# Kernel tuning notes

Hardware: AMD Instinct MI355X
Metric: run time of the kernel (lower is better)

The kernel has to match this reference:

```python
import jax, jax.numpy as jnp
import numpy as np

N_NODES = 500_000
N_EDGES = 16_000_000
N_TYPES = 64


def setup_inputs() -> dict:
    key = jax.random.key(0)
    ks = jax.random.split(key, 8)
    voltage = jax.random.normal(ks[0], (N_NODES,), dtype=jnp.float32)
    stimulus = jax.random.normal(ks[1], (N_NODES,), dtype=jnp.float32)
    neuron_type = jax.random.randint(ks[2], (N_NODES,), 0, N_TYPES, dtype=jnp.int64)
    edge_index = jax.random.randint(ks[3], (2, N_EDGES), 0, N_NODES, dtype=jnp.int64)
    w = jax.random.normal(ks[4], (N_EDGES,), dtype=jnp.float32)
    V_i_rest = jax.random.normal(ks[5], (N_NODES,), dtype=jnp.float32)
    # tau must be positive (divisor); shift uniform away from zero
    tau_i = jax.random.uniform(ks[6], (N_NODES,), dtype=jnp.float32) + 0.5
    # multiple_ReLU per-type scale, abs(1 + 0.5*randn) as in the module
    type_params = jnp.abs(1.0 + 0.5 * jax.random.normal(ks[7], (N_TYPES, 1), dtype=jnp.float32))
    return {
        "voltage": voltage,
        "stimulus": stimulus,
        "neuron_type": neuron_type,
        "edge_index": edge_index,
        "w": w,
        "V_i_rest": V_i_rest,
        "tau_i": tau_i,
        "type_params": type_params,
    }


def reference(voltage, stimulus, neuron_type, edge_index, w, V_i_rest, tau_i, type_params):
    # voltage: (N,), edge_index: (2,E), w: (E,), type_params: (T,1)
    v = voltage[:, None]  # (N,1)
    src = edge_index[0]
    dst = edge_index[1]
    # per-edge message: w_e * relu(v_src) * param[type(src)]   -> (E,1)
    edge_msg = w[:, None] * jax.nn.relu(v[src]) * type_params[neuron_type[src]]
    # scatter_add to destination nodes -> (N,1)
    msg = jax.ops.segment_sum(edge_msg, dst, num_segments=v.shape[0])
    # dv/dt = (-v + msg + e + v_rest) / tau
    dv = (-v + msg + stimulus[:, None] + V_i_rest[:, None]) / tau_i[:, None]
    return dv
```

## Files before the change

### kernel.cpp

```cpp
#include <hip/hip_runtime.h>


#define BSHIFT 10
#define BSIZE  1024
#define NBMAX  512
#define GPB    4096
#define EPB    (GPB * 4)


__global__ void pre_g_kernel(const float* __restrict__ v,
                             const int* __restrict__ ntype,
                             const float* __restrict__ tp,
                             float* __restrict__ g, int n) {
    int i = blockIdx.x * blockDim.x + threadIdx.x;
    if (i < n) {
        float x = v[i];
        x = x > 0.0f ? x : 0.0f;
        g[i] = x * tp[ntype[i]];
    }
}

__global__ __launch_bounds__(1024, 8)
void scatter_kernel(const int* __restrict__ src,
                    const int* __restrict__ dst,
                    const float* __restrict__ w,
                    const float* __restrict__ g,
                    unsigned* __restrict__ sorted,
                    unsigned* __restrict__ lpref_g,
                    int G, int n_edges, int nblk, int nb) {
    __shared__ unsigned stage[EPB];
    __shared__ unsigned lstart[NBMAX];
    __shared__ unsigned lcur[NBMAX];
    __shared__ unsigned wsum[16];
    int blk = blockIdx.x, tid = threadIdx.x;
    int wid = tid >> 6, lane = tid & 63;
    bool last = (blk == nblk - 1);

    if (tid < NBMAX) lcur[tid] = 0;
    __syncthreads();

    const int4*   s4 = (const int4*)src;
    const int4*   d4 = (const int4*)dst;
    const float4* w4 = (const float4*)w;
    int gstart = blk * GPB;
    int gend = gstart + GPB; if (gend > G) gend = G;

    int4 dreg[4];
    #pragma unroll
    for (int k = 0; k < 4; k++) {
        int i = gstart + tid + k * 1024;
        if (i < gend) {
            int4 d = d4[i];
            dreg[k] = d;
            atomicAdd(&lcur[((unsigned)d.x) >> BSHIFT], 1u);
            atomicAdd(&lcur[((unsigned)d.y) >> BSHIFT], 1u);
            atomicAdd(&lcur[((unsigned)d.z) >> BSHIFT], 1u);
            atomicAdd(&lcur[((unsigned)d.w) >> BSHIFT], 1u);
        }
    }
    if (last) {
        for (int i = G * 4 + tid; i < n_edges; i += 1024)
            atomicAdd(&lcur[((unsigned)dst[i]) >> BSHIFT], 1u);
    }
    __syncthreads();

    unsigned cntv = (tid < NBMAX) ? lcur[tid] : 0u;
    unsigned inc = cntv;
    #pragma unroll
    for (int o = 1; o < 64; o <<= 1) {
        unsigned t = __shfl_up(inc, o, 64);
        if (lane >= o) inc += t;
    }
    if (lane == 63) wsum[wid] = inc;
    __syncthreads();
    if (tid < 64) {
        unsigned x = (lane < 16) ? wsum[lane] : 0u;
        unsigned xi = x;
        #pragma unroll
        for (int o = 1; o < 16; o <<= 1) {
            unsigned t = __shfl_up(xi, o, 64);
            if (lane >= o) xi += t;
        }
        if (lane < 16) wsum[lane] = xi - x;
    }
    __syncthreads();
    if (tid < NBMAX) {
        unsigned excl = inc - cntv + wsum[wid];
        lstart[tid] = excl;
        lcur[tid] = excl;
    }
    __syncthreads();

    #pragma unroll
    for (int k = 0; k < 4; k++) {
        int i = gstart + tid + k * 1024;
        if (i < gend) {
            int4 s = s4[i]; float4 wv = w4[i]; int4 d = dreg[k];
            {
                unsigned b = ((unsigned)d.x) >> BSHIFT;
                unsigned pos = atomicAdd(&lcur[b], 1u);
                stage[pos] = (__float_as_uint(wv.x * g[s.x]) & ~(unsigned)(BSIZE - 1)) |
                             ((unsigned)d.x & (BSIZE - 1));
            }
            {
                unsigned b = ((unsigned)d.y) >> BSHIFT;
                unsigned pos = atomicAdd(&lcur[b], 1u);
                stage[pos] = (__float_as_uint(wv.y * g[s.y]) & ~(unsigned)(BSIZE - 1)) |
                             ((unsigned)d.y & (BSIZE - 1));
            }
            {
                unsigned b = ((unsigned)d.z) >> BSHIFT;
                unsigned pos = atomicAdd(&lcur[b], 1u);
                stage[pos] = (__float_as_uint(wv.z * g[s.z]) & ~(unsigned)(BSIZE - 1)) |
                             ((unsigned)d.z & (BSIZE - 1));
            }
            {
                unsigned b = ((unsigned)d.w) >> BSHIFT;
                unsigned pos = atomicAdd(&lcur[b], 1u);
                stage[pos] = (__float_as_uint(wv.w * g[s.w]) & ~(unsigned)(BSIZE - 1)) |
                             ((unsigned)d.w & (BSIZE - 1));
            }
        }
    }
    if (last) {
        for (int i = G * 4 + tid; i < n_edges; i += 1024) {
            int dd = dst[i];
            unsigned b = ((unsigned)dd) >> BSHIFT;
            unsigned pos = atomicAdd(&lcur[b], 1u);
            stage[pos] = (__float_as_uint(w[i] * g[src[i]]) & ~(unsigned)(BSIZE - 1)) |
                         ((unsigned)dd & (BSIZE - 1));
        }
    }
    __syncthreads();

    unsigned count = (unsigned)(gend > gstart ? (gend - gstart) * 4 : 0) +
                     (last ? (unsigned)(n_edges - G * 4) : 0u);
    uint4* out4 = (uint4*)(sorted + (size_t)blk * EPB);
    const uint4* st4 = (const uint4*)stage;
    unsigned nq = (count + 3u) >> 2;
    for (unsigned i = tid; i < nq; i += 1024) out4[i] = st4[i];

    unsigned* row = lpref_g + (size_t)blk * (nb + 1);
    if (tid < (unsigned)nb)       row[tid] = lstart[tid];
    else if (tid == (unsigned)nb) row[nb]  = count;
}

__global__ __launch_bounds__(512, 8)
void accum_kernel(const unsigned* __restrict__ sorted,
                  const unsigned* __restrict__ lpref_g,
                  const float* __restrict__ v,
                  const float* __restrict__ stim,
                  const float* __restrict__ vrest,
                  const float* __restrict__ tau,
                  float* __restrict__ out,
                  int n_nodes, int nblk, int nb) {
    __shared__ float acc[BSIZE];
    int b = blockIdx.x, tid = threadIdx.x;
    acc[tid] = 0.0f;
    acc[tid + 512] = 0.0f;
    __syncthreads();
    int wave = tid >> 6, lane = tid & 63;
    int rowlen = nb + 1;
    for (int base = wave * 64; base < nblk; base += 8 * 64) {
        int myslice = base + lane;
        unsigned s = 0, e = 0;
        if (myslice < nblk) {
            const unsigned* row = lpref_g + (size_t)myslice * rowlen + b;
            s = row[0];
            e = row[1];
        }
        int kmax = nblk - base; if (kmax > 64) kmax = 64;
        for (int k = 0; k < kmax; k++) {
            unsigned sv = __shfl(s, k, 64);
            unsigned ev = __shfl(e, k, 64);
            const unsigned* seg = sorted + (size_t)(base + k) * EPB;
            for (unsigned j = sv + lane; j < ev; j += 64) {
                unsigned u = seg[j];
                atomicAdd(&acc[u & (BSIZE - 1)],
                          __uint_as_float(u & ~(unsigned)(BSIZE - 1)));
            }
        }
    }
    __syncthreads();
    int i0 = (b << BSHIFT) + tid;
    if (i0 < n_nodes)
        out[i0] = (-v[i0] + acc[tid] + stim[i0] + vrest[i0]) / tau[i0];
    int i1 = i0 + 512;
    if (i1 < n_nodes)
        out[i1] = (-v[i1] + acc[tid + 512] + stim[i1] + vrest[i1]) / tau[i1];
}


__global__ void node_pre_kernel(const float* __restrict__ v,
                                const int* __restrict__ ntype,
                                const float* __restrict__ tp,
                                float* __restrict__ g,
                                float* __restrict__ msg, int n) {
    int i = blockIdx.x * blockDim.x + threadIdx.x;
    if (i < n) {
        float x = v[i];
        x = x > 0.0f ? x : 0.0f;
        g[i] = x * tp[ntype[i]];
        msg[i] = 0.0f;
    }
}

__global__ void edge_scatter_kernel(const int* __restrict__ src,
                                    const int* __restrict__ dst,
                                    const float* __restrict__ w,
                                    const float* __restrict__ g,
                                    float* __restrict__ msg, int n_vec) {
    int i = blockIdx.x * blockDim.x + threadIdx.x;
    if (i < n_vec) {
        int4 s = ((const int4*)src)[i];
        int4 d = ((const int4*)dst)[i];
        float4 wv = ((const float4*)w)[i];
        atomicAdd(&msg[d.x], wv.x * g[s.x]);
        atomicAdd(&msg[d.y], wv.y * g[s.y]);
        atomicAdd(&msg[d.z], wv.z * g[s.z]);
        atomicAdd(&msg[d.w], wv.w * g[s.w]);
    }
}

__global__ void edge_scatter_tail(const int* __restrict__ src,
                                  const int* __restrict__ dst,
                                  const float* __restrict__ w,
                                  const float* __restrict__ g,
                                  float* __restrict__ msg,
                                  int start, int n_edges) {
    int i = start + blockIdx.x * blockDim.x + threadIdx.x;
    if (i < n_edges) atomicAdd(&msg[dst[i]], w[i] * g[src[i]]);
}

__global__ void node_post_kernel(const float* __restrict__ v,
                                 const float* __restrict__ msg,
                                 const float* __restrict__ stim,
                                 const float* __restrict__ vrest,
                                 const float* __restrict__ tau,
                                 float* __restrict__ out, int n) {
    int i = blockIdx.x * blockDim.x + threadIdx.x;
    if (i < n)
        out[i] = (-v[i] + msg[i] + stim[i] + vrest[i]) / tau[i];
}


extern "C" void kernel_launch(void* const* d_in, const int* in_sizes, int n_in,
                              void* d_out, int out_size, void* d_ws, size_t ws_size,
                              hipStream_t stream) {
    const float* voltage  = (const float*)d_in[0];
    const float* stimulus = (const float*)d_in[1];
    const int*   ntype    = (const int*)d_in[2];
    const int*   edge_idx = (const int*)d_in[3];
    const float* w        = (const float*)d_in[4];
    const float* vrest    = (const float*)d_in[5];
    const float* tau      = (const float*)d_in[6];
    const float* tp       = (const float*)d_in[7];
    float* out = (float*)d_out;

    const int n_nodes = in_sizes[0];
    const int n_edges = in_sizes[4];
    const int* src = edge_idx;
    const int* dst = edge_idx + n_edges;

    const int B = 256;
    const int G = n_edges / 4;
    int nblk = (G + GPB - 1) / GPB;
    if (nblk < 1) nblk = 1;
    const int nb = (n_nodes + BSIZE - 1) / BSIZE;

    auto align256 = [](size_t x) { return (x + 255) & ~(size_t)255; };
    size_t g_off      = 0;
    size_t sorted_off = align256(g_off + (size_t)n_nodes * 4);
    size_t lpref_off  = align256(sorted_off + (size_t)nblk * EPB * 4);
    size_t need       = align256(lpref_off + (size_t)nblk * (nb + 1) * 4);

    if (nb < NBMAX && ws_size >= need) {
        float*    g      = (float*)((char*)d_ws + g_off);
        unsigned* sorted = (unsigned*)((char*)d_ws + sorted_off);
        unsigned* lpref  = (unsigned*)((char*)d_ws + lpref_off);

        pre_g_kernel<<<(n_nodes + B - 1) / B, B, 0, stream>>>(
            voltage, ntype, tp, g, n_nodes);
        scatter_kernel<<<nblk, 1024, 0, stream>>>(
            src, dst, w, g, sorted, lpref, G, n_edges, nblk, nb);
        accum_kernel<<<nb, 512, 0, stream>>>(
            sorted, lpref, voltage, stimulus, vrest, tau, out,
            n_nodes, nblk, nb);
    } else {
        float* g   = (float*)d_ws;
        float* msg = (float*)d_ws + n_nodes;
        node_pre_kernel<<<(n_nodes + B - 1) / B, B, 0, stream>>>(
            voltage, ntype, tp, g, msg, n_nodes);
        if (G > 0)
            edge_scatter_kernel<<<(G + B - 1) / B, B, 0, stream>>>(
                src, dst, w, g, msg, G);
        if (G * 4 < n_edges) {
            int rem = n_edges - G * 4;
            edge_scatter_tail<<<(rem + B - 1) / B, B, 0, stream>>>(
                src, dst, w, g, msg, G * 4, n_edges);
        }
        node_post_kernel<<<(n_nodes + B - 1) / B, B, 0, stream>>>(
            voltage, msg, stimulus, vrest, tau, out, n_nodes);
    }
}
```

Measured before the change: 420.8 us.

## Scatter edges into global per-bucket buffers via atomic reservation, simplify accumulation

```diff
diff --git a/kernel.cpp b/kernel.cpp
--- a/kernel.cpp
+++ b/kernel.cpp
@@ -6,18 +6,22 @@
 #define NBMAX  512
 #define GPB    4096
 #define EPB    (GPB * 4)
+#define SPILL_CAP 131072
 
 
 __global__ void pre_g_kernel(const float* __restrict__ v,
                              const int* __restrict__ ntype,
                              const float* __restrict__ tp,
-                             float* __restrict__ g, int n) {
+                             float* __restrict__ g,
+                             unsigned* __restrict__ gcur,
+                             int n, int nb) {
     int i = blockIdx.x * blockDim.x + threadIdx.x;
     if (i < n) {
         float x = v[i];
         x = x > 0.0f ? x : 0.0f;
         g[i] = x * tp[ntype[i]];
     }
+    if (i <= nb) gcur[i] = 0u;
 }
 
 __global__ __launch_bounds__(1024, 8)
@@ -25,12 +29,14 @@
                     const int* __restrict__ dst,
                     const float* __restrict__ w,
                     const float* __restrict__ g,
-                    unsigned* __restrict__ sorted,
-                    unsigned* __restrict__ lpref_g,
-                    int G, int n_edges, int nblk, int nb) {
+                    unsigned* __restrict__ bucketbuf,
+                    unsigned* __restrict__ gcur,
+                    uint2* __restrict__ spill,
+                    int G, int n_edges, int nblk, int nb, int cap) {
     __shared__ unsigned stage[EPB];
     __shared__ unsigned lstart[NBMAX];
     __shared__ unsigned lcur[NBMAX];
+    __shared__ unsigned gposs[NBMAX];
     __shared__ unsigned wsum[16];
     int blk = blockIdx.x, tid = threadIdx.x;
     int wid = tid >> 6, lane = tid & 63;
@@ -133,61 +139,89 @@
     }
     __syncthreads();
 
-    unsigned count = (unsigned)(gend > gstart ? (gend - gstart) * 4 : 0) +
-                     (last ? (unsigned)(n_edges - G * 4) : 0u);
-    uint4* out4 = (uint4*)(sorted + (size_t)blk * EPB);
-    const uint4* st4 = (const uint4*)stage;
-    unsigned nq = (count + 3u) >> 2;
-    for (unsigned i = tid; i < nq; i += 1024) out4[i] = st4[i];
-
-    unsigned* row = lpref_g + (size_t)blk * (nb + 1);
-    if (tid < (unsigned)nb)       row[tid] = lstart[tid];
-    else if (tid == (unsigned)nb) row[nb]  = count;
-}
-
-__global__ __launch_bounds__(512, 8)
-void accum_kernel(const unsigned* __restrict__ sorted,
-                  const unsigned* __restrict__ lpref_g,
+    if (tid < nb) {
+        unsigned len = lcur[tid] - lstart[tid];
+        unsigned p = 0u;
+        if (len) {
+            p = atomicAdd(&gcur[tid], len);
+            if (p + len > (unsigned)cap) {
+                atomicSub(&gcur[tid], len);
+                unsigned sp = atomicAdd(&gcur[nb], len);
+                p = 0x80000000u | sp;
+            }
+        }
+        gposs[tid] = p;
+    }
+    __syncthreads();
+
+    for (int b = wid; b < nb; b += 16) {
+        unsigned st  = lstart[b];
+        unsigned len = lcur[b] - st;
+        if (!len) continue;
+        unsigned p = gposs[b];
+        if (p & 0x80000000u) {
+            unsigned sp = p & 0x7FFFFFFFu;
+            for (unsigned j = lane; j < len; j += 64) {
+                if (sp + j < SPILL_CAP) {
+                    unsigned u = stage[st + j];
+                    spill[sp + j] = make_uint2(((unsigned)b << BSHIFT) | (u & (BSIZE - 1u)),
+                                               u & ~(unsigned)(BSIZE - 1));
+                }
+            }
+        } else {
+            unsigned* dp = bucketbuf + (size_t)b * (unsigned)cap + p;
+            for (unsigned j = lane; j < len; j += 64)
+                dp[j] = stage[st + j];
+        }
+    }
+}
+
+__global__ __launch_bounds__(1024, 2)
+void accum_kernel(const unsigned* __restrict__ bucketbuf,
+                  const unsigned* __restrict__ gcur,
+                  const uint2* __restrict__ spill,
                   const float* __restrict__ v,
                   const float* __restrict__ stim,
                   const float* __restrict__ vrest,
                   const float* __restrict__ tau,
                   float* __restrict__ out,
-                  int n_nodes, int nblk, int nb) {
+                  int n_nodes, int nb, int cap) {
     __shared__ float acc[BSIZE];
     int b = blockIdx.x, tid = threadIdx.x;
     acc[tid] = 0.0f;
-    acc[tid + 512] = 0.0f;
-    __syncthreads();
-    int wave = tid >> 6, lane = tid & 63;
-    int rowlen = nb + 1;
-    for (int base = wave * 64; base < nblk; base += 8 * 64) {
-        int myslice = base + lane;
-        unsigned s = 0, e = 0;
-        if (myslice < nblk) {
-            const unsigned* row = lpref_g + (size_t)myslice * rowlen + b;
-            s = row[0];
-            e = row[1];
-        }
-        int kmax = nblk - base; if (kmax > 64) kmax = 64;
-        for (int k = 0; k < kmax; k++) {
-            unsigned sv = __shfl(s, k, 64);
-            unsigned ev = __shfl(e, k, 64);
-            const unsigned* seg = sorted + (size_t)(base + k) * EPB;
-            for (unsigned j = sv + lane; j < ev; j += 64) {
-                unsigned u = seg[j];
-                atomicAdd(&acc[u & (BSIZE - 1)],
-                          __uint_as_float(u & ~(unsigned)(BSIZE - 1)));
-            }
-        }
-    }
-    __syncthreads();
+    __syncthreads();
+
+    unsigned cnt = gcur[b];
+    if (cnt > (unsigned)cap) cnt = (unsigned)cap;
+    const unsigned* base = bucketbuf + (size_t)b * (unsigned)cap;
+    const uint4* b4 = (const uint4*)base;
+    unsigned nq = cnt >> 2;
+    for (unsigned i = tid; i < nq; i += 1024) {
+        uint4 u = b4[i];
+        atomicAdd(&acc[u.x & (BSIZE - 1u)], __uint_as_float(u.x & ~(unsigned)(BSIZE - 1)));
+        atomicAdd(&acc[u.y & (BSIZE - 1u)], __uint_as_float(u.y & ~(unsigned)(BSIZE - 1)));
+        atomicAdd(&acc[u.z & (BSIZE - 1u)], __uint_as_float(u.z & ~(unsigned)(BSIZE - 1)));
+        atomicAdd(&acc[u.w & (BSIZE - 1u)], __uint_as_float(u.w & ~(unsigned)(BSIZE - 1)));
+    }
+    for (unsigned i = (nq << 2) + tid; i < cnt; i += 1024) {
+        unsigned u = base[i];
+        atomicAdd(&acc[u & (BSIZE - 1u)], __uint_as_float(u & ~(unsigned)(BSIZE - 1)));
+    }
+
+    unsigned sn = gcur[nb];
+    if (sn) {
+        if (sn > SPILL_CAP) sn = SPILL_CAP;
+        for (unsigned i = tid; i < sn; i += 1024) {
+            uint2 e = spill[i];
+            if ((int)(e.x >> BSHIFT) == b)
+                atomicAdd(&acc[e.x & (BSIZE - 1u)], __uint_as_float(e.y));
+        }
+    }
+    __syncthreads();
+
     int i0 = (b << BSHIFT) + tid;
     if (i0 < n_nodes)
         out[i0] = (-v[i0] + acc[tid] + stim[i0] + vrest[i0]) / tau[i0];
-    int i1 = i0 + 512;
-    if (i1 < n_nodes)
-        out[i1] = (-v[i1] + acc[tid + 512] + stim[i1] + vrest[i1]) / tau[i1];
 }
 
 
@@ -268,24 +302,29 @@
     if (nblk < 1) nblk = 1;
     const int nb = (n_nodes + BSIZE - 1) / BSIZE;
 
+    int cap = (int)(((long long)n_edges * BSIZE) / (long long)(n_nodes > 0 ? n_nodes : 1)) + 2048;
+    cap = (cap + 3) & ~3;
+
     auto align256 = [](size_t x) { return (x + 255) & ~(size_t)255; };
-    size_t g_off      = 0;
-    size_t sorted_off = align256(g_off + (size_t)n_nodes * 4);
-    size_t lpref_off  = align256(sorted_off + (size_t)nblk * EPB * 4);
-    size_t need       = align256(lpref_off + (size_t)nblk * (nb + 1) * 4);
+    size_t g_off     = 0;
+    size_t gcur_off  = align256(g_off + (size_t)n_nodes * 4);
+    size_t spill_off = align256(gcur_off + (size_t)(nb + 1) * 4);
+    size_t bb_off    = align256(spill_off + (size_t)SPILL_CAP * 8);
+    size_t need      = align256(bb_off + (size_t)nb * (size_t)cap * 4);
 
     if (nb < NBMAX && ws_size >= need) {
-        float*    g      = (float*)((char*)d_ws + g_off);
-        unsigned* sorted = (unsigned*)((char*)d_ws + sorted_off);
-        unsigned* lpref  = (unsigned*)((char*)d_ws + lpref_off);
+        float*    g         = (float*)((char*)d_ws + g_off);
+        unsigned* gcur      = (unsigned*)((char*)d_ws + gcur_off);
+        uint2*    spill     = (uint2*)((char*)d_ws + spill_off);
+        unsigned* bucketbuf = (unsigned*)((char*)d_ws + bb_off);
 
         pre_g_kernel<<<(n_nodes + B - 1) / B, B, 0, stream>>>(
-            voltage, ntype, tp, g, n_nodes);
+            voltage, ntype, tp, g, gcur, n_nodes, nb);
         scatter_kernel<<<nblk, 1024, 0, stream>>>(
-            src, dst, w, g, sorted, lpref, G, n_edges, nblk, nb);
-        accum_kernel<<<nb, 512, 0, stream>>>(
-            sorted, lpref, voltage, stimulus, vrest, tau, out,
-            n_nodes, nblk, nb);
+            src, dst, w, g, bucketbuf, gcur, spill, G, n_edges, nblk, nb, cap);
+        accum_kernel<<<nb, 1024, 0, stream>>>(
+            bucketbuf, gcur, spill, voltage, stimulus, vrest, tau, out,
+            n_nodes, nb, cap);
     } else {
         float* g   = (float*)d_ws;
         float* msg = (float*)d_ws + n_nodes;
```

After: 422.7 us. About the same (+0.4%).
